# Kernel tuning notes

Measured on AMD Instinct MI355X. Metric: run time of the kernel, lower is better.

The kernel has to match this reference:

```python
import jax, jax.numpy as jnp
import numpy as np

B = 16            # batch of graphs
N = 512           # n_node
D = 32            # embedding_dim
MAXN = 16         # max_neighbors
E = MAXN * (N - 1)   # 8176 edges per graph
SLEFT = N * D
FSS = 601         # full_support_size
NA = N - 1        # num_actions (so one-hot rows == B*n_node)
IN0 = D + 1       # sa feature dim
NTOT = B * N


def _gat(x, snd, rcv, W, a_src, a_dst, b):
    # single-head GATConv, add_self_loops=False
    h = x @ W                                            # [BN, C]
    e = (h * a_src).sum(-1)[snd] + (h * a_dst).sum(-1)[rcv]
    e = jnp.where(e > 0, e, 0.2 * e)                     # LeakyReLU(0.2)
    m = jax.ops.segment_max(e, rcv, num_segments=NTOT)   # segment softmax
    m = jnp.where(jnp.isfinite(m), m, 0.0)
    ee = jnp.exp(e - m[rcv])
    den = jax.ops.segment_sum(ee, rcv, num_segments=NTOT)
    alpha = ee / (den[rcv] + 1e-16)
    return jax.ops.segment_sum(alpha[:, None] * h[snd], rcv, num_segments=NTOT) + b


def _ln(x, s, o):
    # hk.LayerNorm(axis=-2): normalize over node axis, scale/offset over features
    x3 = x.reshape(B, N, -1)
    mu = x3.mean(axis=1, keepdims=True)
    var = ((x3 - mu) ** 2).mean(axis=1, keepdims=True)
    return ((x3 - mu) * jax.lax.rsqrt(var + 1e-5) * s + o).reshape(B * N, -1)


def _gat_params(key, din, dout):
    k1, k2, k3 = jax.random.split(key, 3)
    sc = 1.0 / np.sqrt(din)
    return (jax.random.normal(k1, (din, dout), jnp.float32) * sc,
            jax.random.normal(k2, (dout,), jnp.float32) * sc,
            jax.random.normal(k3, (dout,), jnp.float32) * sc,
            jnp.zeros((dout,), jnp.float32))


def setup_inputs():
    key = jax.random.key(0)
    ks = jax.random.split(key, 4)
    nodes = jax.random.normal(ks[0], (B, SLEFT), jnp.float32)
    snd = jax.random.randint(ks[1], (B, E), 0, N).astype(jnp.float32)
    rcv = jax.random.randint(ks[2], (B, E), 0, N).astype(jnp.float32)
    ns = jnp.concatenate([nodes, snd, rcv], axis=1)      # [B, SLEFT + 2E]
    a = jax.random.randint(ks[3], (B,), 0, NA + 1)
    inp = {"ns": ns, "a": a}
    dims = [(IN0, 4 * D), (4 * D, 2 * D), (2 * D, 2 * D), (2 * D, D)]
    rdims = [(IN0, FSS), (FSS, FSS), (FSS, FSS), (FSS, FSS)]
    for i, (di, do) in enumerate(dims, 1):
        W, asrc, adst, b = _gat_params(jax.random.fold_in(key, 100 + i), di, do)
        inp.update({f"W{i}": W, f"a{i}s": asrc, f"a{i}d": adst, f"b{i}": b})
        if i < 4:
            inp.update({f"s{i}": jnp.ones((do,), jnp.float32), f"o{i}": jnp.zeros((do,), jnp.float32)})
    for i, (di, do) in enumerate(rdims, 1):
        W, asrc, adst, b = _gat_params(jax.random.fold_in(key, 200 + i), di, do)
        inp.update({f"rW{i}": W, f"ra{i}s": asrc, f"ra{i}d": adst, f"rb{i}": b})
        if i < 4:
            inp.update({f"rs{i}": jnp.ones((FSS,), jnp.float32), f"ro{i}": jnp.zeros((FSS,), jnp.float32)})
    return inp


def reference(ns, a,
              W1, a1s, a1d, b1, s1, o1,
              W2, a2s, a2d, b2, s2, o2,
              W3, a3s, a3d, b3, s3, o3,
              W4, a4s, a4d, b4,
              rW1, ra1s, ra1d, rb1, rs1, ro1,
              rW2, ra2s, ra2d, rb2, rs2, ro2,
              rW3, ra3s, ra3d, rb3, rs3, ro3,
              rW4, ra4s, ra4d, rb4):
    # gbatch: offset per-graph indices into one big graph
    off = (jnp.arange(B, dtype=jnp.int32) * N)[:, None]
    snd = (ns[:, SLEFT:SLEFT + E].astype(jnp.int32) + off).reshape(-1)
    rcv = (ns[:, SLEFT + E:SLEFT + 2 * E].astype(jnp.int32) + off).reshape(-1)
    nodes = ns[:, :SLEFT].reshape(B * N, D)
    sa = jnp.concatenate([nodes, jax.nn.one_hot(a, NA + 1).reshape(-1, 1)], axis=1)
    # reward head
    r = jax.nn.relu(_ln(_gat(sa, snd, rcv, rW1, ra1s, ra1d, rb1), rs1, ro1))
    r = jax.nn.relu(_ln(_gat(r, snd, rcv, rW2, ra2s, ra2d, rb2), rs2, ro2))
    r = jax.nn.relu(_ln(_gat(r, snd, rcv, rW3, ra3s, ra3d, rb3), rs3, ro3))
    r = _gat(r, snd, rcv, rW4, ra4s, ra4d, rb4).reshape(B, N, FSS).sum(axis=1)
    # next-state head
    f = jax.nn.relu(_ln(_gat(sa, snd, rcv, W1, a1s, a1d, b1), s1, o1))
    f = jax.nn.relu(_ln(_gat(f, snd, rcv, W2, a2s, a2d, b2), s2, o2))
    f = jax.nn.relu(_ln(_gat(f, snd, rcv, W3, a3s, a3d, b3), s3, o3))
    f = _gat(f, snd, rcv, W4, a4s, a4d, b4).reshape(B, N * D)
    ns_new = jnp.concatenate([f, ns[:, SLEFT:]], axis=1)
    return (r, ns_new)
```

## Files before the change

### kernel.cpp

```cpp
#include <hip/hip_runtime.h>
#include <math.h>

#define B_ 16
#define N_ 512
#define D_ 32
#define E_ 8176
#define SLEFT_ 16384
#define FSS_ 601
#define BN_ (B_*N_)
#define BE_ (B_*E_)
#define NSROW_ (SLEFT_ + 2*E_)
#define OUT_R_ (B_*FSS_)
#define HLD_ 768

typedef __attribute__((ext_vector_type(8))) short short8;
typedef __attribute__((ext_vector_type(4))) float f32x4;

typedef __attribute__((address_space(3))) uint lds_uint;
typedef __attribute__((address_space(1))) const uint g_uint;

__device__ __forceinline__ void gl_lds16(const ushort* gp, ushort* lp) {
  __builtin_amdgcn_global_load_lds((g_uint*)gp, (lds_uint*)lp, 16, 0, 0);
}

__device__ __forceinline__ ushort f2b(float f) {
  uint u = __builtin_bit_cast(uint, f);
  u += 0x7FFFu + ((u >> 16) & 1u);
  return (ushort)(u >> 16);
}
__device__ __forceinline__ float b2f(ushort h) {
  return __builtin_bit_cast(float, ((uint)h) << 16);
}


__global__ __launch_bounds__(256) void k_indices(const float* __restrict__ ns,
                                                 int* __restrict__ src_i,
                                                 int* __restrict__ dst_i,
                                                 int* __restrict__ cnt) {
  int idx = blockIdx.x*256 + threadIdx.x;
  if (idx >= BE_) return;
  int b = idx / E_;
  int j = idx - b*E_;
  const float* row = ns + (size_t)b*NSROW_;
  int s = (int)row[SLEFT_ + j];
  int r = (int)row[SLEFT_ + E_ + j];
  src_i[idx] = b*N_ + s;
  int dst = b*N_ + r;
  dst_i[idx] = dst;
  atomicAdd(&cnt[dst], 1);
}

__global__ __launch_bounds__(1024) void k_scan(const int* __restrict__ cnt,
                                               int* __restrict__ rowptr) {
  __shared__ int part[1024];
  int t = threadIdx.x;
  int base = t*8;
  int loc[8]; int s = 0;
  #pragma unroll
  for (int i=0;i<8;i++){ loc[i]=cnt[base+i]; s+=loc[i]; }
  part[t]=s; __syncthreads();
  for (int off=1; off<1024; off<<=1) {
    int v = (t>=off)?part[t-off]:0;
    __syncthreads();
    part[t]+=v;
    __syncthreads();
  }
  int ex = (t==0)?0:part[t-1];
  #pragma unroll
  for (int i=0;i<8;i++){ rowptr[base+i]=ex; ex+=loc[i]; }
  if (t==1023) rowptr[BN_]=ex;
}

__global__ __launch_bounds__(256) void k_scatter(const int* __restrict__ src_i,
                                                 const int* __restrict__ dst_i,
                                                 const int* __restrict__ rowptr,
                                                 int* __restrict__ fill,
                                                 int* __restrict__ csr_src) {
  int idx = blockIdx.x*256+threadIdx.x;
  if (idx>=BE_) return;
  int dst = dst_i[idx];
  int pos = rowptr[dst] + atomicAdd(&fill[dst],1);
  csr_src[pos] = src_i[idx];
}


__global__ __launch_bounds__(256) void k_sa(const float* __restrict__ ns,
                                            const int* __restrict__ a,
                                            ushort* __restrict__ sa) {
  int idx = blockIdx.x*256+threadIdx.x;
  if (idx >= BN_*64) return;
  int v = idx >> 6, c = idx & 63;
  int b = v >> 9, n = v & 511;
  float val = 0.f;
  if (c < 32)       val = ns[(size_t)b*NSROW_ + n*32 + c];
  else if (c == 32) val = (a[b]==n) ? 1.f : 0.f;
  sa[idx] = f2b(val);
}


struct WtP { const float* Wr[4]; const float* Wn[4]; ushort* T[4]; };

__global__ __launch_bounds__(256) void k_wt_tr(WtP p) {
  int t = blockIdx.x;
  int s, base, KP, DINR, DINN, DOUTN, KOFF;
  if (t < 48)        { s=0; base=0;    KP=64;  DINR=33;  DINN=33;  DOUTN=128; KOFF=0;   }
  else if (t < 600)  { s=1; base=48;   KP=736; DINR=601; DINN=128; DOUTN=64;  KOFF=608; }
  else if (t < 1104) { s=2; base=600;  KP=672; DINR=601; DINN=64;  DOUTN=64;  KOFF=608; }
  else               { s=3; base=1104; KP=672; DINR=601; DINN=64;  DOUTN=32;  KOFF=608; }
  int ti = t - base;
  int kt = ti / 24, nt = ti - kt*24;
  int k0 = kt*32, n0 = nt*32;
  __shared__ float tile[32][33];
  int tid = threadIdx.x;
  int cc = tid & 31, rr = tid >> 5;
  #pragma unroll
  for (int it=0; it<4; it++) {
    int k = k0 + it*8 + rr;
    int n = n0 + cc;
    float v = 0.f;
    if (n < 640) { if (n < 601 && k < DINR) v = p.Wr[s][(size_t)k*601 + n]; }
    else { int nn = n-640, kk = k-KOFF;
           if (nn < DOUTN && kk >= 0 && kk < DINN) v = p.Wn[s][(size_t)kk*DOUTN + nn]; }
    tile[it*8+rr][cc] = v;
  }
  __syncthreads();
  #pragma unroll
  for (int it=0; it<4; it++) {
    int n = n0 + it*8 + rr;
    int k = k0 + cc;
    p.T[s][(size_t)n*KP + k] = f2b(tile[cc][it*8+rr]);
  }
}


__global__ __launch_bounds__(256) void k_gemm(const ushort* __restrict__ A,
                                              const ushort* __restrict__ Bt,
                                              ushort* __restrict__ C,
                                              float* __restrict__ esed,
                                              const float* __restrict__ asr,
                                              const float* __restrict__ adr,
                                              const float* __restrict__ asn,
                                              const float* __restrict__ adn,
                                              int Kpad, int dn) {
  __shared__ ushort Asm[64*32];
  __shared__ ushort Bsm[128*32];
  int tid = threadIdx.x;
  int rowBase = blockIdx.y * 64;
  int colBase = blockIdx.x * 128;
  int wave = tid >> 6, lane = tid & 63;
  int wr = (wave >> 1) * 32, wc = (wave & 1) * 64;
  int lm = lane & 15, lk = (lane >> 4) * 8;

  f32x4 acc[2][4];
  #pragma unroll
  for (int i=0;i<2;i++)
    #pragma unroll
    for (int j=0;j<4;j++) acc[i][j] = (f32x4){0.f,0.f,0.f,0.f};

  int t0 = tid, t1 = tid + 256;
  const ushort* Ag0 = A  + (size_t)(rowBase + (t0>>2))*Kpad + (t0&3)*8;
  const ushort* Bg0 = Bt + (size_t)(colBase + (t0>>2))*Kpad + (t0&3)*8;
  const ushort* Bg1 = Bt + (size_t)(colBase + (t1>>2))*Kpad + (t1&3)*8;
  ushort* Al0 = &Asm[t0*8];
  ushort* Bl0 = &Bsm[t0*8];
  ushort* Bl1 = &Bsm[t1*8];

  for (int k0 = 0; k0 < Kpad; k0 += 32) {
    gl_lds16(Ag0 + k0, Al0);
    gl_lds16(Bg0 + k0, Bl0);
    gl_lds16(Bg1 + k0, Bl1);
    __syncthreads();
    short8 af[2], bfr[4];
    #pragma unroll
    for (int i=0;i<2;i++) af[i]  = *(short8*)&Asm[(wr + i*16 + lm)*32 + lk];
    #pragma unroll
    for (int j=0;j<4;j++) bfr[j] = *(short8*)&Bsm[(wc + j*16 + lm)*32 + lk];
    #pragma unroll
    for (int i=0;i<2;i++)
      #pragma unroll
      for (int j=0;j<4;j++)
        acc[i][j] = __builtin_amdgcn_mfma_f32_16x16x32_bf16(af[i], bfr[j], acc[i][j], 0,0,0);
    __syncthreads();
  }

  float asv[4], adv[4];
  #pragma unroll
  for (int j=0;j<4;j++) {
    int col = colBase + wc + j*16 + lm;
    float s = 0.f, d = 0.f;
    if (col < 601)      { s = asr[col];     d = adr[col]; }
    else if (col >= 640 && col - 640 < dn) { s = asn[col-640]; d = adn[col-640]; }
    asv[j] = s; adv[j] = d;
  }
  int cr = lane >> 4;
  int ct2 = blockIdx.x*2 + (wc >> 6);
  #pragma unroll
  for (int i=0;i<2;i++) {
    #pragma unroll
    for (int j=0;j<4;j++) {
      int col = colBase + wc + j*16 + lm;
      #pragma unroll
      for (int g=0; g<4; g++) {
        int row = rowBase + wr + i*16 + cr*4 + g;
        C[(size_t)row*HLD_ + col] = f2b(acc[i][j][g]);
      }
    }
    #pragma unroll
    for (int g=0; g<4; g++) {
      float se = 0.f, sd = 0.f;
      #pragma unroll
      for (int j=0;j<4;j++) { se += acc[i][j][g]*asv[j]; sd += acc[i][j][g]*adv[j]; }
      #pragma unroll
      for (int o=1;o<16;o<<=1) { se += __shfl_xor(se,o,64); sd += __shfl_xor(sd,o,64); }
      if (lm == 0) {
        int row = rowBase + wr + i*16 + cr*4 + g;
        esed[(size_t)row*24 + ct2*2 + 0] = se;
        esed[(size_t)row*24 + ct2*2 + 1] = sd;
      }
    }
  }
}


__global__ __launch_bounds__(256) void k_agg(const ushort* __restrict__ h,
                                             const float* __restrict__ esed,
                                             const int* __restrict__ rowptr,
                                             const int* __restrict__ csr,
                                             const float* __restrict__ bias_r,
                                             const float* __restrict__ bias_n,
                                             ushort* __restrict__ g,
                                             int dn) {
  int wid = threadIdx.x>>6, lane = threadIdx.x&63;
  int bid = blockIdx.x;
  int xcd = bid & 7, slot = bid >> 3;
  int graph = xcd + ((slot >> 7) << 3);
  int v = graph*512 + (slot & 127)*4 + wid;
  int s0 = rowptr[v], e0 = rowptr[v+1];
  int deg = e0 - s0;

  float edr = 0.f, edn = 0.f;
  {
    const float* ep = esed + (size_t)v*24;
    #pragma unroll
    for (int t=0;t<10;t++) edr += ep[2*t+1];
    edn = ep[21] + ep[23];
  }

  int ch0 = lane, ch1 = lane + 64;
  bool a1 = ch1 < 96;
  float acc0[8], acc1[8];
  #pragma unroll
  for (int q=0;q<8;q++){ acc0[q]=0.f; acc1[q]=0.f; }

  if (deg <= 64) {
    bool has = lane < deg;
    int u = 0; float er = -__builtin_inff(), en = -__builtin_inff();
    if (has) {
      u = csr[s0 + lane];
      const float* ep = esed + (size_t)u*24;
      float sr = 0.f;
      #pragma unroll
      for (int t=0;t<10;t++) sr += ep[2*t];
      float sn = ep[20] + ep[22];
      er = sr + edr; er = er > 0.f ? er : 0.2f*er;
      en = sn + edn; en = en > 0.f ? en : 0.2f*en;
    }
    float mr = er, mn = en;
    #pragma unroll
    for (int o=32;o;o>>=1) { mr = fmaxf(mr, __shfl_xor(mr,o,64)); mn = fmaxf(mn, __shfl_xor(mn,o,64)); }
    float pr = has ? __expf(er - mr) : 0.f;
    float pn = has ? __expf(en - mn) : 0.f;
    float dr = pr, dnm = pn;
    #pragma unroll
    for (int o=32;o;o>>=1) { dr += __shfl_xor(dr,o,64); dnm += __shfl_xor(dnm,o,64); }
    pr *= 1.f/(dr + 1e-16f);
    pn *= 1.f/(dnm + 1e-16f);

    short8 A0{}, Bv0{}, A1{}, Bv1{};
    float w0r=0.f, w0n=0.f, w1r=0.f, w1n=0.f;
    if (deg > 0) {
      w0r = __shfl(pr, 0, 64); w0n = __shfl(pn, 0, 64); int uu = __shfl(u, 0, 64);
      const ushort* hp = h + (size_t)uu*HLD_;
      A0 = *(const short8*)&hp[ch0*8];
      if (a1) Bv0 = *(const short8*)&hp[ch1*8];
    }
    if (deg > 1) {
      w1r = __shfl(pr, 1, 64); w1n = __shfl(pn, 1, 64); int uu = __shfl(u, 1, 64);
      const ushort* hp = h + (size_t)uu*HLD_;
      A1 = *(const short8*)&hp[ch0*8];
      if (a1) Bv1 = *(const short8*)&hp[ch1*8];
    }
    bool c1r = ch1 < 80;
    for (int t = 0; t < deg; ++t) {
      short8 A2{}, Bv2{}; float w2r=0.f, w2n=0.f;
      if (t+2 < deg) {
        w2r = __shfl(pr, t+2, 64); w2n = __shfl(pn, t+2, 64); int uu = __shfl(u, t+2, 64);
        const ushort* hp = h + (size_t)uu*HLD_;
        A2 = *(const short8*)&hp[ch0*8];
        if (a1) Bv2 = *(const short8*)&hp[ch1*8];
      }
      #pragma unroll
      for (int q=0;q<8;q++) acc0[q] += w0r * b2f((ushort)A0[q]);
      if (a1) {
        float w = c1r ? w0r : w0n;
        #pragma unroll
        for (int q=0;q<8;q++) acc1[q] += w * b2f((ushort)Bv0[q]);
      }
      A0=A1; Bv0=Bv1; w0r=w1r; w0n=w1n;
      A1=A2; Bv1=Bv2; w1r=w2r; w1n=w2n;
    }
  } else {
    float mr = -__builtin_inff(), mn = -__builtin_inff();
    for (int j = s0 + lane; j < e0; j += 64) {
      const float* ep = esed + (size_t)csr[j]*24;
      float sr=0.f; for (int t=0;t<10;t++) sr += ep[2*t];
      float sn = ep[20]+ep[22];
      float er = sr + edr; er = er>0.f?er:0.2f*er;
      float en = sn + edn; en = en>0.f?en:0.2f*en;
      mr = fmaxf(mr, er); mn = fmaxf(mn, en);
    }
    #pragma unroll
    for (int o=32;o;o>>=1) { mr=fmaxf(mr,__shfl_xor(mr,o,64)); mn=fmaxf(mn,__shfl_xor(mn,o,64)); }
    float dr=0.f, dnm=0.f;
    for (int j = s0 + lane; j < e0; j += 64) {
      const float* ep = esed + (size_t)csr[j]*24;
      float sr=0.f; for (int t=0;t<10;t++) sr += ep[2*t];
      float sn = ep[20]+ep[22];
      float er = sr + edr; er = er>0.f?er:0.2f*er;
      float en = sn + edn; en = en>0.f?en:0.2f*en;
      dr += __expf(er-mr); dnm += __expf(en-mn);
    }
    #pragma unroll
    for (int o=32;o;o>>=1) { dr+=__shfl_xor(dr,o,64); dnm+=__shfl_xor(dnm,o,64); }
    float ir = 1.f/(dr+1e-16f), in_ = 1.f/(dnm+1e-16f);
    bool c1r = ch1 < 80;
    for (int j = s0; j < e0; ++j) {
      int uu = csr[j];
      const float* ep = esed + (size_t)uu*24;
      float sr=0.f; for (int t=0;t<10;t++) sr += ep[2*t];
      float sn = ep[20]+ep[22];
      float er = sr + edr; er = er>0.f?er:0.2f*er;
      float en = sn + edn; en = en>0.f?en:0.2f*en;
      float wr2 = __expf(er-mr)*ir, wn2 = __expf(en-mn)*in_;
      const ushort* hp = h + (size_t)uu*HLD_;
      short8 hv = *(const short8*)&hp[ch0*8];
      #pragma unroll
      for (int q=0;q<8;q++) acc0[q] += wr2 * b2f((ushort)hv[q]);
      if (a1) {
        short8 hv2 = *(const short8*)&hp[ch1*8];
        float w = c1r ? wr2 : wn2;
        #pragma unroll
        for (int q=0;q<8;q++) acc1[q] += w * b2f((ushort)hv2[q]);
      }
    }
  }

  ushort* gv = g + (size_t)v*HLD_;
  {
    int cb = ch0*8;
    short8 ov;
    #pragma unroll
    for (int q=0;q<8;q++) ov[q] = (short)f2b(acc0[q] + bias_r[cb+q]);
    *(short8*)&gv[cb] = ov;
  }
  if (a1) {
    int cb = ch1*8;
    short8 ov;
    #pragma unroll
    for (int q=0;q<8;q++) {
      int c = cb+q;
      float val;
      if (c < 601)                         val = acc1[q] + bias_r[c];
      else if (c >= 640 && (c-640) < dn)   val = acc1[q] + bias_n[c-640];
      else                                 val = 0.f;
      ov[q] = (short)f2b(val);
    }
    *(short8*)&gv[cb] = ov;
  }
}


__global__ __launch_bounds__(256) void k_ln_stats(const ushort* __restrict__ g,
                                                  float* __restrict__ st) {
  int b = blockIdx.y, z = blockIdx.z; int n0 = z*64;
  int lc = threadIdx.x & 63, r0 = threadIdx.x >> 6;
  int c = blockIdx.x*64 + lc;
  float s=0.f, q=0.f;
  #pragma unroll 4
  for (int i=0;i<16;i++) {
    int n = n0 + r0*16 + i;
    float x = b2f(g[(size_t)(b*N_+n)*HLD_ + c]);
    s+=x; q+=x*x;
  }
  __shared__ float S[4][64], Q[4][64];
  S[r0][lc]=s; Q[r0][lc]=q; __syncthreads();
  if (r0==0) {
    st[((size_t)(z*2+0)*B_ + b)*HLD_ + c] = S[0][lc]+S[1][lc]+S[2][lc]+S[3][lc];
    st[((size_t)(z*2+1)*B_ + b)*HLD_ + c] = Q[0][lc]+Q[1][lc]+Q[2][lc]+Q[3][lc];
  }
}


__global__ __launch_bounds__(256) void k_ln_apply(const ushort* __restrict__ g,
                                                  const float* __restrict__ st,
                                                  const float* __restrict__ scr,
                                                  const float* __restrict__ ofr,
                                                  const float* __restrict__ scn,
                                                  const float* __restrict__ ofn,
                                                  ushort* __restrict__ xb,
                                                  int dn, int Kpad) {
  int tid = threadIdx.x;
  int pp = blockIdx.x*128 + (tid & 127);
  int c0 = pp*2;
  if (c0 >= Kpad) return;
  int vbase = blockIdx.y*16;
  int b = vbase >> 9;
  float mv[2], av[2];
  #pragma unroll
  for (int q=0;q<2;q++) {
    int c = c0+q;
    int cs; bool valid; float scale, offs;
    if (c < 608) { cs = c; valid = c < 601;
                   scale = valid ? scr[c] : 0.f; offs = valid ? ofr[c] : 0.f; }
    else { int cn = c - 608; cs = 640 + cn; valid = cn < dn;
           scale = valid ? scn[cn] : 0.f; offs = valid ? ofn[cn] : 0.f; }
    float mul = 0.f, add = 0.f;
    if (valid) {
      float s=0.f, qq=0.f;
      #pragma unroll
      for (int z=0;z<8;z++) {
        s  += st[((size_t)(z*2+0)*B_ + b)*HLD_ + cs];
        qq += st[((size_t)(z*2+1)*B_ + b)*HLD_ + cs];
      }
      float mu = s*(1.f/N_);
      float var = qq*(1.f/N_) - mu*mu;
      float rs = rsqrtf(var+1e-5f);
      mul = rs*scale;
      add = offs - mu*rs*scale;
    }
    mv[q] = mul; av[q] = add;
  }
  int cs0 = (c0 < 608) ? c0 : 640 + (c0 - 608);
  for (int i = tid >> 7; i < 16; i += 2) {
    int v = vbase + i;
    uint gg = *(const uint*)&g[(size_t)v*HLD_ + cs0];
    float x0 = b2f((ushort)(gg & 0xFFFFu));
    float x1 = b2f((ushort)(gg >> 16));
    float y0 = x0*mv[0] + av[0]; y0 = y0 > 0.f ? y0 : 0.f;
    float y1 = x1*mv[1] + av[1]; y1 = y1 > 0.f ? y1 : 0.f;
    *(uint*)&xb[(size_t)v*Kpad + c0] = ((uint)f2b(y1) << 16) | f2b(y0);
  }
}


__global__ __launch_bounds__(256) void k_rsum(const ushort* __restrict__ g,
                                              float* __restrict__ rsp) {
  int b = blockIdx.y, z = blockIdx.z; int n0 = z*64;
  int lc = threadIdx.x & 63, r0 = threadIdx.x>>6;
  int c = blockIdx.x*64 + lc;
  float s = 0.f;
  if (c < FSS_) {
    #pragma unroll 4
    for (int i=0;i<16;i++) {
      int n = n0 + r0*16 + i;
      s += b2f(g[(size_t)(b*N_+n)*HLD_ + c]);
    }
  }
  __shared__ float S[4][64];
  S[r0][lc]=s; __syncthreads();
  if (r0==0 && c<FSS_)
    rsp[((size_t)z*B_ + b)*FSS_ + c] = S[0][lc]+S[1][lc]+S[2][lc]+S[3][lc];
}


__global__ __launch_bounds__(256) void k_final(const float* __restrict__ rsp,
                                               const ushort* __restrict__ g,
                                               const float* __restrict__ ns,
                                               float* __restrict__ out) {
  int idx = blockIdx.x*256+threadIdx.x;
  if (idx < OUT_R_) {
    int b = idx / FSS_, c = idx - b*FSS_;
    float s = 0.f;
    #pragma unroll
    for (int z=0;z<8;z++) s += rsp[((size_t)z*B_ + b)*FSS_ + c];
    out[idx] = s;
  } else {
    int j2 = idx - OUT_R_;
    if (j2 >= B_*NSROW_) return;
    int b = j2 / NSROW_; int j = j2 - b*NSROW_;
    float v;
    if (j < SLEFT_) {
      int n = j >> 5, c = j & 31;
      v = b2f(g[(size_t)(b*N_+n)*HLD_ + 640 + c]);
    } else {
      v = ns[(size_t)b*NSROW_ + j];
    }
    out[idx] = v;
  }
}


extern "C" void kernel_launch(void* const* d_in, const int* in_sizes, int n_in,
                              void* d_out, int out_size, void* d_ws, size_t ws_size,
                              hipStream_t stream) {
  const float* ns = (const float*)d_in[0];
  const int*   a  = (const int*)d_in[1];

  const float *W[4], *As[4], *Ad[4], *Bb[4], *Sc[3], *Of[3];
  const float *rW[4], *rAs[4], *rAd[4], *rBb[4], *rSc[3], *rOf[3];
  int p = 2;
  for (int i=0;i<4;i++){
    W[i]=(const float*)d_in[p++]; As[i]=(const float*)d_in[p++];
    Ad[i]=(const float*)d_in[p++]; Bb[i]=(const float*)d_in[p++];
    if (i<3){ Sc[i]=(const float*)d_in[p++]; Of[i]=(const float*)d_in[p++]; }
  }
  for (int i=0;i<4;i++){
    rW[i]=(const float*)d_in[p++]; rAs[i]=(const float*)d_in[p++];
    rAd[i]=(const float*)d_in[p++]; rBb[i]=(const float*)d_in[p++];
    if (i<3){ rSc[i]=(const float*)d_in[p++]; rOf[i]=(const float*)d_in[p++]; }
  }

  char* w = (char*)d_ws;
  auto carve = [&](size_t bytes)->void* {
    void* r = (void*)w;
    w += (bytes + 255) & ~(size_t)255;
    return r;
  };
  ushort* xb   = (ushort*)carve((size_t)BN_*736*2);
  ushort* hbuf = (ushort*)carve((size_t)BN_*HLD_*2);
  ushort* gbuf = (ushort*)carve((size_t)BN_*HLD_*2);
  ushort* sabf = (ushort*)carve((size_t)BN_*64*2);
  float* esed  = (float*)carve((size_t)BN_*24*4);
  float* stp   = (float*)carve((size_t)16*B_*HLD_*4);
  float* rsp   = (float*)carve((size_t)8*B_*FSS_*4);
  int* src_i   = (int*)carve((size_t)BE_*4);
  int* dst_i   = (int*)carve((size_t)BE_*4);
  int* cnt     = (int*)carve((size_t)2*BN_*4);
  int* fill    = cnt + BN_;
  int* rowptr  = (int*)carve((size_t)(BN_+1)*4);
  int* csr_src = (int*)carve((size_t)BE_*4);
  ushort* Wt[4];
  Wt[0] = (ushort*)carve((size_t)768*64*2);
  Wt[1] = (ushort*)carve((size_t)768*736*2);
  Wt[2] = (ushort*)carve((size_t)768*672*2);
  Wt[3] = (ushort*)carve((size_t)768*672*2);

  float* out = (float*)d_out;

  hipMemsetAsync(cnt, 0, (size_t)2*BN_*4, stream);

  k_indices<<<(BE_+255)/256, 256, 0, stream>>>(ns, src_i, dst_i, cnt);
  k_scan<<<1, 1024, 0, stream>>>(cnt, rowptr);
  k_scatter<<<(BE_+255)/256, 256, 0, stream>>>(src_i, dst_i, rowptr, fill, csr_src);
  k_sa<<<(BN_*64+255)/256, 256, 0, stream>>>(ns, a, sabf);

  WtP wtp;
  for (int i=0;i<4;i++){ wtp.Wr[i]=rW[i]; wtp.Wn[i]=W[i]; wtp.T[i]=Wt[i]; }
  k_wt_tr<<<1608, 256, 0, stream>>>(wtp);

  dim3 ggrid(6, BN_/64);

  k_gemm<<<ggrid, 256, 0, stream>>>(sabf, Wt[0], hbuf, esed, rAs[0],rAd[0],As[0],Ad[0], 64, 128);
  k_agg<<<BN_/4, 256, 0, stream>>>(hbuf, esed, rowptr, csr_src, rBb[0], Bb[0], gbuf, 128);
  k_ln_stats<<<dim3(12, B_, 8), 256, 0, stream>>>(gbuf, stp);
  k_ln_apply<<<dim3(3, BN_/16), 256, 0, stream>>>(gbuf, stp, rSc[0],rOf[0],Sc[0],Of[0], xb, 128, 736);

  k_gemm<<<ggrid, 256, 0, stream>>>(xb, Wt[1], hbuf, esed, rAs[1],rAd[1],As[1],Ad[1], 736, 64);
  k_agg<<<BN_/4, 256, 0, stream>>>(hbuf, esed, rowptr, csr_src, rBb[1], Bb[1], gbuf, 64);
  k_ln_stats<<<dim3(12, B_, 8), 256, 0, stream>>>(gbuf, stp);
  k_ln_apply<<<dim3(3, BN_/16), 256, 0, stream>>>(gbuf, stp, rSc[1],rOf[1],Sc[1],Of[1], xb, 64, 672);

  k_gemm<<<ggrid, 256, 0, stream>>>(xb, Wt[2], hbuf, esed, rAs[2],rAd[2],As[2],Ad[2], 672, 64);
  k_agg<<<BN_/4, 256, 0, stream>>>(hbuf, esed, rowptr, csr_src, rBb[2], Bb[2], gbuf, 64);
  k_ln_stats<<<dim3(12, B_, 8), 256, 0, stream>>>(gbuf, stp);
  k_ln_apply<<<dim3(3, BN_/16), 256, 0, stream>>>(gbuf, stp, rSc[2],rOf[2],Sc[2],Of[2], xb, 64, 672);

  k_gemm<<<ggrid, 256, 0, stream>>>(xb, Wt[3], hbuf, esed, rAs[3],rAd[3],As[3],Ad[3], 672, 32);
  k_agg<<<BN_/4, 256, 0, stream>>>(hbuf, esed, rowptr, csr_src, rBb[3], Bb[3], gbuf, 32);

  k_rsum<<<dim3(10, B_, 8), 256, 0, stream>>>(gbuf, rsp);
  k_final<<<(OUT_R_ + B_*NSROW_ + 255)/256, 256, 0, stream>>>(rsp, gbuf, ns, out);
}
```

Baseline: 409.6 us.

## Recast GAT aggregation as dense per-graph attention-matrix GEMM on MFMA

```diff
diff --git a/kernel.cpp b/kernel.cpp
--- a/kernel.cpp
+++ b/kernel.cpp
@@ -133,15 +133,15 @@
 }
 
 
-__global__ __launch_bounds__(256) void k_gemm(const ushort* __restrict__ A,
-                                              const ushort* __restrict__ Bt,
-                                              ushort* __restrict__ C,
-                                              float* __restrict__ esed,
-                                              const float* __restrict__ asr,
-                                              const float* __restrict__ adr,
-                                              const float* __restrict__ asn,
-                                              const float* __restrict__ adn,
-                                              int Kpad, int dn) {
+__global__ __launch_bounds__(256) void k_gemmT(const ushort* __restrict__ Wt,
+                                               const ushort* __restrict__ X,
+                                               ushort* __restrict__ ht,
+                                               float* __restrict__ esed,
+                                               const float* __restrict__ asr,
+                                               const float* __restrict__ adr,
+                                               const float* __restrict__ asn,
+                                               const float* __restrict__ adn,
+                                               int Kpad, int dn) {
   __shared__ ushort Asm[64*32];
   __shared__ ushort Bsm[128*32];
   int tid = threadIdx.x;
@@ -158,9 +158,9 @@
     for (int j=0;j<4;j++) acc[i][j] = (f32x4){0.f,0.f,0.f,0.f};
 
   int t0 = tid, t1 = tid + 256;
-  const ushort* Ag0 = A  + (size_t)(rowBase + (t0>>2))*Kpad + (t0&3)*8;
-  const ushort* Bg0 = Bt + (size_t)(colBase + (t0>>2))*Kpad + (t0&3)*8;
-  const ushort* Bg1 = Bt + (size_t)(colBase + (t1>>2))*Kpad + (t1&3)*8;
+  const ushort* Ag0 = Wt + (size_t)(rowBase + (t0>>2))*Kpad + (t0&3)*8;
+  const ushort* Bg0 = X  + (size_t)(colBase + (t0>>2))*Kpad + (t0&3)*8;
+  const ushort* Bg1 = X  + (size_t)(colBase + (t1>>2))*Kpad + (t1&3)*8;
   ushort* Al0 = &Asm[t0*8];
   ushort* Bl0 = &Bsm[t0*8];
   ushort* Bl1 = &Bsm[t1*8];
@@ -183,17 +183,19 @@
     __syncthreads();
   }
 
-  float asv[4], adv[4];
-  #pragma unroll
-  for (int j=0;j<4;j++) {
-    int col = colBase + wc + j*16 + lm;
-    float s = 0.f, d = 0.f;
-    if (col < 601)      { s = asr[col];     d = adr[col]; }
-    else if (col >= 640 && col - 640 < dn) { s = asn[col-640]; d = adn[col-640]; }
-    asv[j] = s; adv[j] = d;
-  }
   int cr = lane >> 4;
-  int ct2 = blockIdx.x*2 + (wc >> 6);
+  float asv[2][4], adv[2][4];
+  #pragma unroll
+  for (int i=0;i<2;i++)
+    #pragma unroll
+    for (int g=0; g<4; g++) {
+      int r = rowBase + wr + i*16 + cr*4 + g;
+      float s = 0.f, d = 0.f;
+      if (r < 601)                        { s = asr[r];     d = adr[r]; }
+      else if (r >= 640 && r - 640 < dn)  { s = asn[r-640]; d = adn[r-640]; }
+      asv[i][g] = s; adv[i][g] = d;
+    }
+
   #pragma unroll
   for (int i=0;i<2;i++) {
     #pragma unroll
@@ -201,181 +203,167 @@
       int col = colBase + wc + j*16 + lm;
       #pragma unroll
       for (int g=0; g<4; g++) {
-        int row = rowBase + wr + i*16 + cr*4 + g;
-        C[(size_t)row*HLD_ + col] = f2b(acc[i][j][g]);
+        int r = rowBase + wr + i*16 + cr*4 + g;
+        ht[(size_t)r*BN_ + col] = f2b(acc[i][j][g]);
       }
     }
-    #pragma unroll
-    for (int g=0; g<4; g++) {
-      float se = 0.f, sd = 0.f;
+  }
+  float* es = (rowBase < 640) ? esed          : esed + 2*BN_;
+  float* ed = (rowBase < 640) ? esed + BN_    : esed + 3*BN_;
+  #pragma unroll
+  for (int j=0;j<4;j++) {
+    float se = 0.f, sd = 0.f;
+    #pragma unroll
+    for (int i=0;i<2;i++)
       #pragma unroll
-      for (int j=0;j<4;j++) { se += acc[i][j][g]*asv[j]; sd += acc[i][j][g]*adv[j]; }
-      #pragma unroll
-      for (int o=1;o<16;o<<=1) { se += __shfl_xor(se,o,64); sd += __shfl_xor(sd,o,64); }
-      if (lm == 0) {
-        int row = rowBase + wr + i*16 + cr*4 + g;
-        esed[(size_t)row*24 + ct2*2 + 0] = se;
-        esed[(size_t)row*24 + ct2*2 + 1] = sd;
+      for (int g=0; g<4; g++) { se += acc[i][j][g]*asv[i][g]; sd += acc[i][j][g]*adv[i][g]; }
+    se += __shfl_xor(se, 16, 64); se += __shfl_xor(se, 32, 64);
+    sd += __shfl_xor(sd, 16, 64); sd += __shfl_xor(sd, 32, 64);
+    if (cr == 0) {
+      int v = colBase + wc + j*16 + lm;
+      atomicAdd(&es[v], se);
+      atomicAdd(&ed[v], sd);
+    }
+  }
+}
+
+
+__global__ __launch_bounds__(256) void k_pbuild(const float* __restrict__ esed,
+                                                const int* __restrict__ rowptr,
+                                                const int* __restrict__ csr,
+                                                ushort* __restrict__ Pm) {
+  const float* es_r = esed;
+  const float* ed_r = esed + BN_;
+  const float* es_n = esed + 2*BN_;
+  const float* ed_n = esed + 3*BN_;
+  int wid = threadIdx.x>>6, lane = threadIdx.x&63;
+  int v = blockIdx.x*4 + wid;
+  int s0 = rowptr[v], e0 = rowptr[v+1];
+  float edr = ed_r[v], edn = ed_n[v];
+
+  float mr = -__builtin_inff(), mn = -__builtin_inff();
+  for (int c0 = s0; c0 < e0; c0 += 64) {
+    int j = c0 + lane;
+    float er = -__builtin_inff(), en = -__builtin_inff();
+    if (j < e0) {
+      int u = csr[j];
+      er = es_r[u] + edr; er = er > 0.f ? er : 0.2f*er;
+      en = es_n[u] + edn; en = en > 0.f ? en : 0.2f*en;
+    }
+    mr = fmaxf(mr, er); mn = fmaxf(mn, en);
+  }
+  #pragma unroll
+  for (int o=32;o;o>>=1) { mr = fmaxf(mr, __shfl_xor(mr,o,64)); mn = fmaxf(mn, __shfl_xor(mn,o,64)); }
+
+  float accr[8], accn[8];
+  #pragma unroll
+  for (int q=0;q<8;q++){ accr[q]=0.f; accn[q]=0.f; }
+  float denr = 0.f, denn = 0.f;
+  for (int c0 = s0; c0 < e0; c0 += 64) {
+    int j = c0 + lane;
+    int u = 0; float pwr = 0.f, pwn = 0.f;
+    if (j < e0) {
+      u = csr[j];
+      float er = es_r[u] + edr; er = er > 0.f ? er : 0.2f*er;
+      float en = es_n[u] + edn; en = en > 0.f ? en : 0.2f*en;
+      pwr = __expf(er - mr);
+      pwn = __expf(en - mn);
+    }
+    denr += pwr; denn += pwn;
+    int cl = e0 - c0; if (cl > 64) cl = 64;
+    for (int t = 0; t < cl; ++t) {
+      float pr = __shfl(pwr, t, 64);
+      float pn = __shfl(pwn, t, 64);
+      int   uu = __shfl(u,   t, 64);
+      int rel = (uu & 511) - (lane<<3);
+      if (rel >= 0 && rel < 8) {
+        #pragma unroll
+        for (int q=0;q<8;q++) if (rel==q) { accr[q] += pr; accn[q] += pn; }
       }
     }
   }
-}
-
-
-__global__ __launch_bounds__(256) void k_agg(const ushort* __restrict__ h,
-                                             const float* __restrict__ esed,
-                                             const int* __restrict__ rowptr,
-                                             const int* __restrict__ csr,
-                                             const float* __restrict__ bias_r,
-                                             const float* __restrict__ bias_n,
-                                             ushort* __restrict__ g,
-                                             int dn) {
-  int wid = threadIdx.x>>6, lane = threadIdx.x&63;
+  #pragma unroll
+  for (int o=32;o;o>>=1) { denr += __shfl_xor(denr,o,64); denn += __shfl_xor(denn,o,64); }
+  float scr = 1.f/(denr + 1e-16f);
+  float scn = 1.f/(denn + 1e-16f);
+  short8 ovr, ovn;
+  #pragma unroll
+  for (int q=0;q<8;q++) { ovr[q] = (short)f2b(accr[q]*scr); ovn[q] = (short)f2b(accn[q]*scn); }
+  *(short8*)&Pm[(size_t)v*1024 + lane*8]       = ovr;
+  *(short8*)&Pm[(size_t)v*1024 + 512 + lane*8] = ovn;
+}
+
+
+__global__ __launch_bounds__(256) void k_pgemm(const ushort* __restrict__ Pm,
+                                               const ushort* __restrict__ ht,
+                                               ushort* __restrict__ g,
+                                               const float* __restrict__ bias_r,
+                                               const float* __restrict__ bias_n,
+                                               int dn) {
+  __shared__ ushort Asm[64*32];
+  __shared__ ushort Bsm[128*32];
   int bid = blockIdx.x;
   int xcd = bid & 7, slot = bid >> 3;
-  int graph = xcd + ((slot >> 7) << 3);
-  int v = graph*512 + (slot & 127)*4 + wid;
-  int s0 = rowptr[v], e0 = rowptr[v+1];
-  int deg = e0 - s0;
-
-  float edr = 0.f, edn = 0.f;
-  {
-    const float* ep = esed + (size_t)v*24;
-    #pragma unroll
-    for (int t=0;t<10;t++) edr += ep[2*t+1];
-    edn = ep[21] + ep[23];
-  }
-
-  int ch0 = lane, ch1 = lane + 64;
-  bool a1 = ch1 < 96;
-  float acc0[8], acc1[8];
-  #pragma unroll
-  for (int q=0;q<8;q++){ acc0[q]=0.f; acc1[q]=0.f; }
-
-  if (deg <= 64) {
-    bool has = lane < deg;
-    int u = 0; float er = -__builtin_inff(), en = -__builtin_inff();
-    if (has) {
-      u = csr[s0 + lane];
-      const float* ep = esed + (size_t)u*24;
-      float sr = 0.f;
+  int graph = xcd + 8*(slot/48);
+  int idx = slot % 48;
+  int bx = idx % 6, rt = idx / 6;
+  int rowBase = graph*512 + rt*64;
+  int colBase = bx*128;
+  int headoff = (bx == 5) ? 512 : 0;
+  int tid = threadIdx.x;
+  int wave = tid >> 6, lane = tid & 63;
+  int wr = (wave >> 1) * 32, wc = (wave & 1) * 64;
+  int lm = lane & 15, lk = (lane >> 4) * 8;
+
+  f32x4 acc[2][4];
+  #pragma unroll
+  for (int i=0;i<2;i++)
+    #pragma unroll
+    for (int j=0;j<4;j++) acc[i][j] = (f32x4){0.f,0.f,0.f,0.f};
+
+  int t0 = tid, t1 = tid + 256;
+  const ushort* Ag0 = Pm + (size_t)(rowBase + (t0>>2))*1024 + headoff + (t0&3)*8;
+  const ushort* Bg0 = ht + (size_t)(colBase + (t0>>2))*BN_ + graph*512 + (t0&3)*8;
+  const ushort* Bg1 = ht + (size_t)(colBase + (t1>>2))*BN_ + graph*512 + (t1&3)*8;
+  ushort* Al0 = &Asm[t0*8];
+  ushort* Bl0 = &Bsm[t0*8];
+  ushort* Bl1 = &Bsm[t1*8];
+
+  for (int k0 = 0; k0 < 512; k0 += 32) {
+    gl_lds16(Ag0 + k0, Al0);
+    gl_lds16(Bg0 + k0, Bl0);
+    gl_lds16(Bg1 + k0, Bl1);
+    __syncthreads();
+    short8 af[2], bfr[4];
+    #pragma unroll
+    for (int i=0;i<2;i++) af[i]  = *(short8*)&Asm[(wr + i*16 + lm)*32 + lk];
+    #pragma unroll
+    for (int j=0;j<4;j++) bfr[j] = *(short8*)&Bsm[(wc + j*16 + lm)*32 + lk];
+    #pragma unroll
+    for (int i=0;i<2;i++)
       #pragma unroll
-      for (int t=0;t<10;t++) sr += ep[2*t];
-      float sn = ep[20] + ep[22];
-      er = sr + edr; er = er > 0.f ? er : 0.2f*er;
-      en = sn + edn; en = en > 0.f ? en : 0.2f*en;
-    }
-    float mr = er, mn = en;
-    #pragma unroll
-    for (int o=32;o;o>>=1) { mr = fmaxf(mr, __shfl_xor(mr,o,64)); mn = fmaxf(mn, __shfl_xor(mn,o,64)); }
-    float pr = has ? __expf(er - mr) : 0.f;
-    float pn = has ? __expf(en - mn) : 0.f;
-    float dr = pr, dnm = pn;
-    #pragma unroll
-    for (int o=32;o;o>>=1) { dr += __shfl_xor(dr,o,64); dnm += __shfl_xor(dnm,o,64); }
-    pr *= 1.f/(dr + 1e-16f);
-    pn *= 1.f/(dnm + 1e-16f);
-
-    short8 A0{}, Bv0{}, A1{}, Bv1{};
-    float w0r=0.f, w0n=0.f, w1r=0.f, w1n=0.f;
-    if (deg > 0) {
-      w0r = __shfl(pr, 0, 64); w0n = __shfl(pn, 0, 64); int uu = __shfl(u, 0, 64);
-      const ushort* hp = h + (size_t)uu*HLD_;
-      A0 = *(const short8*)&hp[ch0*8];
-      if (a1) Bv0 = *(const short8*)&hp[ch1*8];
-    }
-    if (deg > 1) {
-      w1r = __shfl(pr, 1, 64); w1n = __shfl(pn, 1, 64); int uu = __shfl(u, 1, 64);
-      const ushort* hp = h + (size_t)uu*HLD_;
-      A1 = *(const short8*)&hp[ch0*8];
-      if (a1) Bv1 = *(const short8*)&hp[ch1*8];
-    }
-    bool c1r = ch1 < 80;
-    for (int t = 0; t < deg; ++t) {
-      short8 A2{}, Bv2{}; float w2r=0.f, w2n=0.f;
-      if (t+2 < deg) {
-        w2r = __shfl(pr, t+2, 64); w2n = __shfl(pn, t+2, 64); int uu = __shfl(u, t+2, 64);
-        const ushort* hp = h + (size_t)uu*HLD_;
-        A2 = *(const short8*)&hp[ch0*8];
-        if (a1) Bv2 = *(const short8*)&hp[ch1*8];
+      for (int j=0;j<4;j++)
+        acc[i][j] = __builtin_amdgcn_mfma_f32_16x16x32_bf16(af[i], bfr[j], acc[i][j], 0,0,0);
+    __syncthreads();
+  }
+
+  int cr = lane >> 4;
+  #pragma unroll
+  for (int i=0;i<2;i++) {
+    #pragma unroll
+    for (int j=0;j<4;j++) {
+      int col = colBase + wc + j*16 + lm;
+      float bv; bool valid;
+      if (col < 601)                        { bv = bias_r[col];     valid = true; }
+      else if (col >= 640 && col-640 < dn)  { bv = bias_n[col-640]; valid = true; }
+      else                                  { bv = 0.f;             valid = false; }
+      #pragma unroll
+      for (int gg=0; gg<4; gg++) {
+        int v = rowBase + wr + i*16 + cr*4 + gg;
+        float val = valid ? acc[i][j][gg] + bv : 0.f;
+        g[(size_t)v*HLD_ + col] = f2b(val);
       }
-      #pragma unroll
-      for (int q=0;q<8;q++) acc0[q] += w0r * b2f((ushort)A0[q]);
-      if (a1) {
-        float w = c1r ? w0r : w0n;
-        #pragma unroll
-        for (int q=0;q<8;q++) acc1[q] += w * b2f((ushort)Bv0[q]);
-      }
-      A0=A1; Bv0=Bv1; w0r=w1r; w0n=w1n;
-      A1=A2; Bv1=Bv2; w1r=w2r; w1n=w2n;
-    }
-  } else {
-    float mr = -__builtin_inff(), mn = -__builtin_inff();
-    for (int j = s0 + lane; j < e0; j += 64) {
-      const float* ep = esed + (size_t)csr[j]*24;
-      float sr=0.f; for (int t=0;t<10;t++) sr += ep[2*t];
-      float sn = ep[20]+ep[22];
-      float er = sr + edr; er = er>0.f?er:0.2f*er;
-      float en = sn + edn; en = en>0.f?en:0.2f*en;
-      mr = fmaxf(mr, er); mn = fmaxf(mn, en);
-    }
-    #pragma unroll
-    for (int o=32;o;o>>=1) { mr=fmaxf(mr,__shfl_xor(mr,o,64)); mn=fmaxf(mn,__shfl_xor(mn,o,64)); }
-    float dr=0.f, dnm=0.f;
-    for (int j = s0 + lane; j < e0; j += 64) {
-      const float* ep = esed + (size_t)csr[j]*24;
-      float sr=0.f; for (int t=0;t<10;t++) sr += ep[2*t];
-      float sn = ep[20]+ep[22];
-      float er = sr + edr; er = er>0.f?er:0.2f*er;
-      float en = sn + edn; en = en>0.f?en:0.2f*en;
-      dr += __expf(er-mr); dnm += __expf(en-mn);
-    }
-    #pragma unroll
-    for (int o=32;o;o>>=1) { dr+=__shfl_xor(dr,o,64); dnm+=__shfl_xor(dnm,o,64); }
-    float ir = 1.f/(dr+1e-16f), in_ = 1.f/(dnm+1e-16f);
-    bool c1r = ch1 < 80;
-    for (int j = s0; j < e0; ++j) {
-      int uu = csr[j];
-      const float* ep = esed + (size_t)uu*24;
-      float sr=0.f; for (int t=0;t<10;t++) sr += ep[2*t];
-      float sn = ep[20]+ep[22];
-      float er = sr + edr; er = er>0.f?er:0.2f*er;
-      float en = sn + edn; en = en>0.f?en:0.2f*en;
-      float wr2 = __expf(er-mr)*ir, wn2 = __expf(en-mn)*in_;
-      const ushort* hp = h + (size_t)uu*HLD_;
-      short8 hv = *(const short8*)&hp[ch0*8];
-      #pragma unroll
-      for (int q=0;q<8;q++) acc0[q] += wr2 * b2f((ushort)hv[q]);
-      if (a1) {
-        short8 hv2 = *(const short8*)&hp[ch1*8];
-        float w = c1r ? wr2 : wn2;
-        #pragma unroll
-        for (int q=0;q<8;q++) acc1[q] += w * b2f((ushort)hv2[q]);
-      }
-    }
-  }
-
-  ushort* gv = g + (size_t)v*HLD_;
-  {
-    int cb = ch0*8;
-    short8 ov;
-    #pragma unroll
-    for (int q=0;q<8;q++) ov[q] = (short)f2b(acc0[q] + bias_r[cb+q]);
-    *(short8*)&gv[cb] = ov;
-  }
-  if (a1) {
-    int cb = ch1*8;
-    short8 ov;
-    #pragma unroll
-    for (int q=0;q<8;q++) {
-      int c = cb+q;
-      float val;
-      if (c < 601)                         val = acc1[q] + bias_r[c];
-      else if (c >= 640 && (c-640) < dn)   val = acc1[q] + bias_n[c-640];
-      else                                 val = 0.f;
-      ov[q] = (short)f2b(val);
-    }
-    *(short8*)&gv[cb] = ov;
+    }
   }
 }
 
@@ -527,10 +515,11 @@
     return r;
   };
   ushort* xb   = (ushort*)carve((size_t)BN_*736*2);
-  ushort* hbuf = (ushort*)carve((size_t)BN_*HLD_*2);
+  ushort* ht   = (ushort*)carve((size_t)HLD_*BN_*2);
   ushort* gbuf = (ushort*)carve((size_t)BN_*HLD_*2);
+  ushort* Pm   = (ushort*)carve((size_t)BN_*1024*2);
   ushort* sabf = (ushort*)carve((size_t)BN_*64*2);
-  float* esed  = (float*)carve((size_t)BN_*24*4);
+  float* esed  = (float*)carve((size_t)4*BN_*4);
   float* stp   = (float*)carve((size_t)16*B_*HLD_*4);
   float* rsp   = (float*)carve((size_t)8*B_*FSS_*4);
   int* src_i   = (int*)carve((size_t)BE_*4);
@@ -558,25 +547,25 @@
   for (int i=0;i<4;i++){ wtp.Wr[i]=rW[i]; wtp.Wn[i]=W[i]; wtp.T[i]=Wt[i]; }
   k_wt_tr<<<1608, 256, 0, stream>>>(wtp);
 
-  dim3 ggrid(6, BN_/64);
-
-  k_gemm<<<ggrid, 256, 0, stream>>>(sabf, Wt[0], hbuf, esed, rAs[0],rAd[0],As[0],Ad[0], 64, 128);
-  k_agg<<<BN_/4, 256, 0, stream>>>(hbuf, esed, rowptr, csr_src, rBb[0], Bb[0], gbuf, 128);
-  k_ln_stats<<<dim3(12, B_, 8), 256, 0, stream>>>(gbuf, stp);
-  k_ln_apply<<<dim3(3, BN_/16), 256, 0, stream>>>(gbuf, stp, rSc[0],rOf[0],Sc[0],Of[0], xb, 128, 736);
-
-  k_gemm<<<ggrid, 256, 0, stream>>>(xb, Wt[1], hbuf, esed, rAs[1],rAd[1],As[1],Ad[1], 736, 64);
-  k_agg<<<BN_/4, 256, 0, stream>>>(hbuf, esed, rowptr, csr_src, rBb[1], Bb[1], gbuf, 64);
-  k_ln_stats<<<dim3(12, B_, 8), 256, 0, stream>>>(gbuf, stp);
-  k_ln_apply<<<dim3(3, BN_/16), 256, 0, stream>>>(gbuf, stp, rSc[1],rOf[1],Sc[1],Of[1], xb, 64, 672);
-
-  k_gemm<<<ggrid, 256, 0, stream>>>(xb, Wt[2], hbuf, esed, rAs[2],rAd[2],As[2],Ad[2], 672, 64);
-  k_agg<<<BN_/4, 256, 0, stream>>>(hbuf, esed, rowptr, csr_src, rBb[2], Bb[2], gbuf, 64);
-  k_ln_stats<<<dim3(12, B_, 8), 256, 0, stream>>>(gbuf, stp);
-  k_ln_apply<<<dim3(3, BN_/16), 256, 0, stream>>>(gbuf, stp, rSc[2],rOf[2],Sc[2],Of[2], xb, 64, 672);
-
-  k_gemm<<<ggrid, 256, 0, stream>>>(xb, Wt[3], hbuf, esed, rAs[3],rAd[3],As[3],Ad[3], 672, 32);
-  k_agg<<<BN_/4, 256, 0, stream>>>(hbuf, esed, rowptr, csr_src, rBb[3], Bb[3], gbuf, 32);
+  dim3 tg(64, 12);
+
+  const ushort* xin[4] = { sabf, xb, xb, xb };
+  int Kp[4] = { 64, 736, 672, 672 };
+  int dns[4] = { 128, 64, 64, 32 };
+
+  for (int L=0; L<4; ++L) {
+    hipMemsetAsync(esed, 0, (size_t)4*BN_*4, stream);
+    k_gemmT<<<tg, 256, 0, stream>>>(Wt[L], xin[L], ht, esed,
+                                    rAs[L], rAd[L], As[L], Ad[L], Kp[L], dns[L]);
+    k_pbuild<<<BN_/4, 256, 0, stream>>>(esed, rowptr, csr_src, Pm);
+    k_pgemm<<<768, 256, 0, stream>>>(Pm, ht, gbuf, rBb[L], Bb[L], dns[L]);
+    if (L < 3) {
+      k_ln_stats<<<dim3(12, B_, 8), 256, 0, stream>>>(gbuf, stp);
+      int Kpn = (L==0) ? 736 : 672;
+      k_ln_apply<<<dim3(3, BN_/16), 256, 0, stream>>>(gbuf, stp,
+                  rSc[L], rOf[L], Sc[L], Of[L], xb, dns[L], Kpn);
+    }
+  }
 
   k_rsum<<<dim3(10, B_, 8), 256, 0, stream>>>(gbuf, rsp);
   k_final<<<(OUT_R_ + B_*NSROW_ + 255)/256, 256, 0, stream>>>(rsp, gbuf, ns, out);
```

After: 418.5 us. 1.02x slower.
